# Optimization experiments

Hardware: AMD Instinct MI355X
Metric: run time of the kernel (lower is better)

## Reference

```python
import jax, jax.numpy as jnp
import numpy as np

D = 1024      # input_dim
H = 4096      # hidden_dim
E = 8         # expert_count
TOP_K = 2
N = 8192      # tokens
LN_EPS = 1e-5


def setup_inputs() -> dict:
    key = jax.random.key(0)
    ks = jax.random.split(key, 10)
    s_d = 1.0 / np.sqrt(D)
    s_h = 1.0 / np.sqrt(H)
    return {
        "x": jax.random.normal(ks[0], (N, D), dtype=jnp.float32),
        "ln_gamma": jnp.ones((D,), jnp.float32),
        "ln_beta": jnp.zeros((D,), jnp.float32),
        "conf_w": jax.random.uniform(ks[1], (D, 1), jnp.float32, -s_d, s_d),
        "conf_b": jnp.zeros((1,), jnp.float32),
        "router_w": jax.random.uniform(ks[2], (D, E), jnp.float32, -s_d, s_d),
        "router_b": jnp.zeros((E,), jnp.float32),
        "w1": jax.random.uniform(ks[3], (E, D, H), jnp.float32, -s_d, s_d),
        "b1": jax.random.uniform(ks[4], (E, H), jnp.float32, -s_d, s_d),
        "w2": jax.random.uniform(ks[5], (E, H, D), jnp.float32, -s_h, s_h),
        "b2": jax.random.uniform(ks[6], (E, D), jnp.float32, -s_h, s_h),
    }


def reference(x, ln_gamma, ln_beta, conf_w, conf_b, router_w, router_b, w1, b1, w2, b2):
    # LayerNorm (torch default eps=1e-5, affine)
    mu = jnp.mean(x, axis=-1, keepdims=True)
    var = jnp.mean(jnp.square(x - mu), axis=-1, keepdims=True)
    x_norm = (x - mu) * jax.lax.rsqrt(var + LN_EPS) * ln_gamma + ln_beta

    # layer-skip confidence head
    confidence = jax.nn.sigmoid(x_norm @ conf_w + conf_b)  # [N,1]

    # router: softmax -> top-k -> renormalize selected weights
    router_probs = jax.nn.softmax(x_norm @ router_w + router_b, axis=-1)  # [N,E]
    vals, indices = jax.lax.top_k(router_probs, TOP_K)                    # [N,K]
    vals = vals / jnp.sum(vals, axis=-1, keepdims=True)

    # scatter top-k weights into dense per-expert combine weights [N,E]
    combine_w = jnp.zeros((x.shape[0], E), x.dtype).at[
        jnp.arange(x.shape[0])[:, None], indices].add(vals)

    # dispatch/combine: loop over small fixed expert count (dense compute,
    # weighted by combine_w, mathematically identical to per-token dispatch)
    combined = jnp.zeros_like(x)
    for e in range(E):
        h = jax.nn.relu(x_norm @ w1[e] + b1[e])      # [N,H]
        combined = combined + combine_w[:, e:e + 1] * (h @ w2[e] + b2[e])

    output = x + combined
    return output, confidence, x
```

## Files before the change

kernel.cpp:

```cpp
#include <hip/hip_runtime.h>
#include <hip/hip_bf16.h>

#define N_TOK 8192
#define DIM   1024
#define HID   4096
#define NEXP  8
#define CSTR  64
#define RTMAX 136
#define HROWS 16896
#define EPS   264

using bf16x8 = __attribute__((ext_vector_type(8))) short;
using f32x4  = __attribute__((ext_vector_type(4))) float;

__device__ __forceinline__ void gload_lds16(const void* g, void* l) {
  __builtin_amdgcn_global_load_lds(
      (const __attribute__((address_space(1))) unsigned int*)g,
      (__attribute__((address_space(3))) unsigned int*)l, 16, 0, 0);
}

__device__ __forceinline__ float wredsum(float v) {
#pragma unroll
  for (int off = 32; off > 0; off >>= 1) v += __shfl_xor(v, off, 64);
  return v;
}

__device__ __forceinline__ unsigned short f2bf(float f) {
  __hip_bfloat16 h = __float2bfloat16(f);
  return *reinterpret_cast<unsigned short*>(&h);
}
__device__ __forceinline__ float bf2f(unsigned short u) {
  return __uint_as_float((unsigned)u << 16);
}

__device__ __forceinline__ void transpose_body(
    const float* __restrict__ src, __hip_bfloat16* __restrict__ dst,
    int R, int C, int c0, int r0, float (*tile)[65]) {
  const int tid = threadIdx.x;
  const int tx = tid & 15, ty = tid >> 4;
#pragma unroll
  for (int k = 0; k < 4; k++) {
    const int row = ty + k * 16;
    const float4 v = *(const float4*)(src + (size_t)(r0 + row) * C + c0 + tx * 4);
    tile[row][tx * 4 + 0] = v.x; tile[row][tx * 4 + 1] = v.y;
    tile[row][tx * 4 + 2] = v.z; tile[row][tx * 4 + 3] = v.w;
  }
  __syncthreads();
#pragma unroll
  for (int k = 0; k < 4; k++) {
    const int orow = ty + k * 16;
    ushort4 st;
    st.x = f2bf(tile[tx * 4 + 0][orow]);
    st.y = f2bf(tile[tx * 4 + 1][orow]);
    st.z = f2bf(tile[tx * 4 + 2][orow]);
    st.w = f2bf(tile[tx * 4 + 3][orow]);
    *(ushort4*)((unsigned short*)dst + (size_t)(c0 + orow) * R + r0 + tx * 4) = st;
  }
}

__global__ __launch_bounds__(256) void setup_kernel(
    const float* __restrict__ x, const float* __restrict__ gamma, const float* __restrict__ beta,
    const float* __restrict__ conf_w, const float* __restrict__ conf_b,
    const float* __restrict__ rw, const float* __restrict__ rb,
    const float* __restrict__ w1, const float* __restrict__ w2,
    __hip_bfloat16* __restrict__ w1t, __hip_bfloat16* __restrict__ w2t,
    __hip_bfloat16* __restrict__ xn, float* __restrict__ out,
    int* __restrict__ counts, int* __restrict__ lists, float* __restrict__ wts,
    int2* __restrict__ idx) {
  __shared__ float tile[64][65];
  const int b = (int)blockIdx.x;
  if (b < 8192) {
    const int z = b >> 10, r = b & 1023;
    const int cx = r & 63, ry = r >> 6;
    transpose_body(w1 + (size_t)z * DIM * HID, w1t + (size_t)z * DIM * HID,
                   DIM, HID, cx * 64, ry * 64, tile);
    return;
  }
  if (b < 16384) {
    const int bb = b - 8192;
    const int z = bb >> 10, r = bb & 1023;
    const int cx = r & 15, ry = r >> 4;
    transpose_body(w2 + (size_t)z * HID * DIM, w2t + (size_t)z * HID * DIM,
                   HID, DIM, cx * 64, ry * 64, tile);
    return;
  }
  const int t = (b - 16384) * 4 + ((int)threadIdx.x >> 6);
  const int lane = threadIdx.x & 63;
  const float* xr = x + (size_t)t * DIM;

  float4 xv[4];
#pragma unroll
  for (int q = 0; q < 4; q++) xv[q] = *(const float4*)(xr + q * 256 + lane * 4);

  float s = 0.f, s2 = 0.f;
#pragma unroll
  for (int q = 0; q < 4; q++) {
    s  += xv[q].x + xv[q].y + xv[q].z + xv[q].w;
    s2 += xv[q].x * xv[q].x + xv[q].y * xv[q].y + xv[q].z * xv[q].z + xv[q].w * xv[q].w;
  }
  s = wredsum(s); s2 = wredsum(s2);
  const float mu  = s * (1.f / DIM);
  const float inv = rsqrtf(s2 * (1.f / DIM) - mu * mu + 1e-5f);

  float p[9];
#pragma unroll
  for (int e = 0; e < 9; e++) p[e] = 0.f;

#pragma unroll
  for (int q = 0; q < 4; q++) {
    const int d0 = q * 256 + lane * 4;
    const float4 g4 = *(const float4*)(gamma + d0);
    const float4 b4 = *(const float4*)(beta + d0);
    float v0 = (xv[q].x - mu) * inv * g4.x + b4.x;
    float v1 = (xv[q].y - mu) * inv * g4.y + b4.y;
    float v2 = (xv[q].z - mu) * inv * g4.z + b4.z;
    float v3 = (xv[q].w - mu) * inv * g4.w + b4.w;

    ushort4 st; st.x = f2bf(v0); st.y = f2bf(v1); st.z = f2bf(v2); st.w = f2bf(v3);
    *(ushort4*)((unsigned short*)xn + (size_t)t * DIM + d0) = st;
    *(float4*)(out + (size_t)t * DIM + d0) = xv[q];
    *(float4*)(out + (size_t)N_TOK * DIM + N_TOK + (size_t)t * DIM + d0) = xv[q];

    const float vv[4] = {v0, v1, v2, v3};
#pragma unroll
    for (int j = 0; j < 4; j++) {
      const int d = d0 + j;
      const float v = vv[j];
      p[8] += v * conf_w[d];
      const float4 r0 = *(const float4*)(rw + d * 8);
      const float4 r1 = *(const float4*)(rw + d * 8 + 4);
      p[0] += v * r0.x; p[1] += v * r0.y; p[2] += v * r0.z; p[3] += v * r0.w;
      p[4] += v * r1.x; p[5] += v * r1.y; p[6] += v * r1.z; p[7] += v * r1.w;
    }
  }
#pragma unroll
  for (int e = 0; e < 9; e++) p[e] = wredsum(p[e]);

  if (lane == 0) {
    float L[8];
#pragma unroll
    for (int e = 0; e < 8; e++) L[e] = p[e] + rb[e];
    const float cl = p[8] + conf_b[0];
    out[(size_t)N_TOK * DIM + t] = 1.f / (1.f + expf(-cl));

    float mx = L[0];
#pragma unroll
    for (int e = 1; e < 8; e++) mx = fmaxf(mx, L[e]);
    float pe[8];
#pragma unroll
    for (int e = 0; e < 8; e++) pe[e] = expf(L[e] - mx);
    int i0 = 0; float v0 = pe[0];
#pragma unroll
    for (int e = 1; e < 8; e++) if (pe[e] > v0) { v0 = pe[e]; i0 = e; }
    int i1 = -1; float v1 = -1.f;
#pragma unroll
    for (int e = 0; e < 8; e++) if (e != i0 && pe[e] > v1) { v1 = pe[e]; i1 = e; }
    const float wsum = v0 + v1;
    const float w0 = v0 / wsum, w1v = v1 / wsum;
    int p0 = atomicAdd(&counts[i0 * CSTR], 1);
    lists[i0 * N_TOK + p0] = t; wts[i0 * N_TOK + p0] = w0;
    int p1 = atomicAdd(&counts[i1 * CSTR], 1);
    lists[i1 * N_TOK + p1] = t; wts[i1 * N_TOK + p1] = w1v;
    idx[t] = make_int2((i0 << 13) | p0, (i1 << 13) | p1);
  }
}

__global__ void bases_kernel(const int* __restrict__ counts, int* __restrict__ bases,
                             int* __restrict__ meta) {
  if (threadIdx.x == 0) {
    int s = 0, r = 0;
#pragma unroll
    for (int e = 0; e < NEXP; e++) {
      bases[e] = s; meta[e] = r;
      const int c = counts[e * CSTR];
      s += c; r += (c + 127) >> 7;
    }
    meta[NEXP] = r;
  }
}


#define GEMM_CORE(NT)                                                                   \
  f32x4 acc[4][4] = {};                                                                 \
  stage(0, 0); stage(1, 24576);                                                         \
  for (int t = 0; t < (NT); ++t) {                                                      \
    const int pb = (t % 3) * 24576;                                                     \
    if (t + 1 < (NT)) { asm volatile("s_waitcnt vmcnt(3)" ::: "memory"); }              \
    else              { asm volatile("s_waitcnt vmcnt(0)" ::: "memory"); }              \
    __builtin_amdgcn_s_barrier();                                                       \
    if (t + 2 < (NT)) stage(t + 2, ((t + 2) % 3) * 24576);                              \
    const char* Ab = smem + pb + Abase;                                                 \
    const char* Bb = smem + pb + Bbase;                                                 \
    bf16x8 bfr[4], afr[4];                                                              \
    _Pragma("unroll")                                                                   \
    for (int n = 0; n < 4; n++) bfr[n] = *(const bf16x8*)(Bb + n * 1024);               \
    _Pragma("unroll")                                                                   \
    for (int m = 0; m < 4; m++) afr[m] = *(const bf16x8*)(Ab + m * 1024);               \
    asm volatile("s_waitcnt lgkmcnt(0)" ::: "memory");                                  \
    __builtin_amdgcn_sched_barrier(0);                                                  \
    __builtin_amdgcn_s_setprio(1);                                                      \
    _Pragma("unroll")                                                                   \
    for (int m = 0; m < 4; m++)                                                         \
      _Pragma("unroll")                                                                 \
      for (int n = 0; n < 4; n++)                                                       \
        acc[m][n] = __builtin_amdgcn_mfma_f32_16x16x32_bf16(afr[m], bfr[n], acc[m][n], 0, 0, 0); \
    __builtin_amdgcn_s_setprio(0);                                                      \
  }

#define DECODE_BLOCK(PPX)                                                     \
  int panel, rtg;                                                             \
  if ((PPX) > 0) {                                                            \
    const int x_ = (int)blockIdx.x & 7;                                       \
    const int q_ = (int)blockIdx.x >> 3;                                      \
    rtg = q_ / (PPX);                                                         \
    panel = x_ * (PPX) + (q_ - rtg * (PPX));                                  \
  } else {                                                                    \
    panel = (int)blockIdx.x / RTMAX;                                          \
    rtg = (int)blockIdx.x - panel * RTMAX;                                    \
  }                                                                           \
  if (rtg >= meta[NEXP]) return;                                              \
  int e = 0;                                                                  \
  _Pragma("unroll")                                                           \
  for (int k = 1; k < NEXP; k++) if (meta[k] <= rtg) e = k;                   \
  const int rt = rtg - meta[e];                                               \
  const int cnt = counts[e * CSTR];                                           \
  const int hbase = bases[e];

#define GEMM_COMMON()                                                         \
  __shared__ char smem[73728];                                                \
  const int tid = threadIdx.x;                                                \
  const int l = tid & 63;                                                     \
  const int w8 = tid >> 6;                                                    \
  const int wr = w8 >> 2;                                                     \
  const int wc = w8 & 3;                                                      \
  const int lr = l & 15;                                                      \
  const int pchunk = (l >> 4) ^ ((lr >> 1) & 3);                              \
  const int Abase = (wr * 64 + lr) * 64 + pchunk * 16;                        \
  const int Bbase = 8192 + (wc * 64 + lr) * 64 + pchunk * 16;                 \
  const int srow = tid >> 2;                      \
  const int lc = (tid & 3) ^ ((srow >> 1) & 3);

#define EPILOGUE(EXPR, DSTROW)                                                \
  __builtin_amdgcn_s_barrier();                                               \
  {                                                                           \
    unsigned short* ep = (unsigned short*)smem;                               \
    _Pragma("unroll")                                                         \
    for (int n = 0; n < 4; n++) {                                             \
      const int col = wc * 64 + n * 16 + lr;                                  \
      _Pragma("unroll")                                                       \
      for (int m = 0; m < 4; m++) {                                           \
        f32x4 v = acc[m][n];                                                  \
        _Pragma("unroll")                                                     \
        for (int j = 0; j < 4; j++) {                                         \
          const int row = wr * 64 + m * 16 + (l >> 4) * 4 + j;                \
          ep[row * EPS + col] = (EXPR);                                       \
        }                                                                     \
      }                                                                       \
    }                                                                         \
    asm volatile("s_waitcnt lgkmcnt(0)" ::: "memory");                        \
    __builtin_amdgcn_s_barrier();                                             \
    const int g = tid >> 5, u = tid & 31;                                     \
    _Pragma("unroll")                                                         \
    for (int i = 0; i < 8; i++) {                                             \
      const int row = i * 16 + g;                                             \
      const int pos = rt * 128 + row;                                         \
      if (pos < cnt) {                                                        \
        bf16x8 vv = *(const bf16x8*)(ep + row * EPS + u * 8);                 \
        *(bf16x8*)(DSTROW + u * 8) = vv;                                      \
      }                                                                       \
    }                                                                         \
  }

__global__ __launch_bounds__(512, 4) void gemm1_kernel(
    const __hip_bfloat16* __restrict__ xn, const __hip_bfloat16* __restrict__ w1t_b,
    const float* __restrict__ b1, const int* __restrict__ lists,
    const int* __restrict__ counts, const int* __restrict__ bases,
    const int* __restrict__ meta, __hip_bfloat16* __restrict__ hbuf, const int ppx) {
  DECODE_BLOCK(ppx)
  const int ct = panel;
  const int* list = lists + e * N_TOK;
  const __hip_bfloat16* w1t = w1t_b + (size_t)e * DIM * HID;
  GEMM_COMMON()

  const int apos = rt * 128 + srow;
  const int tok = list[apos < cnt ? apos : 0];
  const unsigned short* srcA0 = (const unsigned short*)xn + (size_t)tok * DIM + lc * 8;
  const unsigned short* srcB0 = (const unsigned short*)w1t + (size_t)(ct * 256 + srow) * DIM + lc * 8;
  const unsigned short* srcB1 = (const unsigned short*)w1t + (size_t)(ct * 256 + 128 + srow) * DIM + lc * 8;

  auto stage = [&](int tt, int lbase) {
    gload_lds16(srcA0 + tt * 32, smem + lbase + tid * 16);
    gload_lds16(srcB0 + tt * 32, smem + lbase + 8192 + tid * 16);
    gload_lds16(srcB1 + tt * 32, smem + lbase + 16384 + tid * 16);
  };

  GEMM_CORE(DIM / 32)

  const float bv[4] = {
    b1[e * HID + ct * 256 + wc * 64 + 0 * 16 + lr],
    b1[e * HID + ct * 256 + wc * 64 + 1 * 16 + lr],
    b1[e * HID + ct * 256 + wc * 64 + 2 * 16 + lr],
    b1[e * HID + ct * 256 + wc * 64 + 3 * 16 + lr]};
#pragma unroll
  for (int n = 0; n < 4; n++)
#pragma unroll
    for (int m = 0; m < 4; m++)
#pragma unroll
      for (int j = 0; j < 4; j++) acc[m][n][j] = fmaxf(acc[m][n][j] + bv[n], 0.f);
  EPILOGUE(f2bf(v[j]),
           (unsigned short*)hbuf + (size_t)(hbase + pos) * HID + ct * 256)
}

__global__ __launch_bounds__(512, 4) void gemm2_kernel(
    const __hip_bfloat16* __restrict__ hbuf, const __hip_bfloat16* __restrict__ w2t_b,
    const int* __restrict__ counts, const int* __restrict__ bases,
    const int* __restrict__ meta, __hip_bfloat16* __restrict__ ybuf,
    const int SK, const int ppx) {
  DECODE_BLOCK(ppx)
  const int ct = panel & 3;
  const int ksp = panel >> 2;
  const int kbase = ksp * (HID / SK);
  const __hip_bfloat16* w2t = w2t_b + (size_t)e * DIM * HID;
  GEMM_COMMON()

  const unsigned short* srcA0 = (const unsigned short*)hbuf +
      (size_t)(hbase + rt * 128 + srow) * HID + kbase + lc * 8;
  const unsigned short* srcB0 = (const unsigned short*)w2t +
      (size_t)(ct * 256 + srow) * HID + kbase + lc * 8;
  const unsigned short* srcB1 = (const unsigned short*)w2t +
      (size_t)(ct * 256 + 128 + srow) * HID + kbase + lc * 8;

  auto stage = [&](int tt, int lbase) {
    gload_lds16(srcA0 + tt * 32, smem + lbase + tid * 16);
    gload_lds16(srcB0 + tt * 32, smem + lbase + 8192 + tid * 16);
    gload_lds16(srcB1 + tt * 32, smem + lbase + 16384 + tid * 16);
  };

  const int nk = (HID / 32) / SK;
  GEMM_CORE(nk)

  EPILOGUE(f2bf(v[j]),
           (unsigned short*)ybuf + ((size_t)ksp * HROWS + hbase + pos) * DIM + ct * 256)
}

__global__ __launch_bounds__(256) void combine_kernel(
    const __hip_bfloat16* __restrict__ ybuf, const float* __restrict__ b2,
    const int2* __restrict__ idx, const float* __restrict__ wv,
    const int* __restrict__ bases, float* __restrict__ out, const int SK) {
  const int t = blockIdx.x * 4 + (threadIdx.x >> 6);
  const int lane = threadIdx.x & 63;
  const int2 iv = idx[t];
  const int e0 = iv.x >> 13, p0 = iv.x & (N_TOK - 1);
  const int e1 = iv.y >> 13, p1 = iv.y & (N_TOK - 1);
  const float w0 = wv[iv.x], w1 = wv[iv.y];
  const int r0 = bases[e0] + p0;
  const int r1 = bases[e1] + p1;
#pragma unroll
  for (int q = 0; q < 4; q++) {
    const int d0 = q * 256 + lane * 4;
    float4 o = *(const float4*)(out + (size_t)t * DIM + d0);
    float y0x = 0.f, y0y = 0.f, y0z = 0.f, y0w = 0.f;
    float y1x = 0.f, y1y = 0.f, y1z = 0.f, y1w = 0.f;
    for (int s = 0; s < SK; s++) {
      const ushort4 a = *(const ushort4*)((const unsigned short*)ybuf +
                          ((size_t)s * HROWS + r0) * DIM + d0);
      const ushort4 b = *(const ushort4*)((const unsigned short*)ybuf +
                          ((size_t)s * HROWS + r1) * DIM + d0);
      y0x += bf2f(a.x); y0y += bf2f(a.y); y0z += bf2f(a.z); y0w += bf2f(a.w);
      y1x += bf2f(b.x); y1y += bf2f(b.y); y1z += bf2f(b.z); y1w += bf2f(b.w);
    }
    const float4 bb0 = *(const float4*)(b2 + e0 * DIM + d0);
    const float4 bb1 = *(const float4*)(b2 + e1 * DIM + d0);
    o.x += w0 * (y0x + bb0.x) + w1 * (y1x + bb1.x);
    o.y += w0 * (y0y + bb0.y) + w1 * (y1y + bb1.y);
    o.z += w0 * (y0z + bb0.z) + w1 * (y1z + bb1.z);
    o.w += w0 * (y0w + bb0.w) + w1 * (y1w + bb1.w);
    *(float4*)(out + (size_t)t * DIM + d0) = o;
  }
}

extern "C" void kernel_launch(void* const* d_in, const int* in_sizes, int n_in,
                              void* d_out, int out_size, void* d_ws, size_t ws_size,
                              hipStream_t stream) {
  (void)in_sizes; (void)n_in; (void)out_size;
  const float* x      = (const float*)d_in[0];
  const float* gamma  = (const float*)d_in[1];
  const float* beta   = (const float*)d_in[2];
  const float* conf_w = (const float*)d_in[3];
  const float* conf_b = (const float*)d_in[4];
  const float* rw     = (const float*)d_in[5];
  const float* rb     = (const float*)d_in[6];
  const float* w1     = (const float*)d_in[7];
  const float* b1     = (const float*)d_in[8];
  const float* w2     = (const float*)d_in[9];
  const float* b2     = (const float*)d_in[10];
  float* out = (float*)d_out;

  char* w = (char*)d_ws;
  auto alloc = [&](size_t bytes) { char* p = w; w += (bytes + 255) & ~255ULL; return p; };

  __hip_bfloat16* xn = (__hip_bfloat16*)alloc((size_t)N_TOK * DIM * 2);
  int*   lists  = (int*)alloc((size_t)NEXP * N_TOK * 4);
  float* wtsb   = (float*)alloc((size_t)NEXP * N_TOK * 4);
  int*   counts = (int*)alloc(NEXP * CSTR * 4);
  int*   bases  = (int*)alloc(256);
  int*   meta   = (int*)alloc(256);
  int2*  idx    = (int2*)alloc((size_t)N_TOK * 8);

  const size_t hbufA = (size_t)HROWS * HID * 2;
  const size_t wtA   = (size_t)NEXP * DIM * HID * 2;
  __hip_bfloat16* hbuf = (__hip_bfloat16*)alloc(hbufA);
  __hip_bfloat16* w1t  = (__hip_bfloat16*)alloc(wtA);
  __hip_bfloat16* w2t  = (__hip_bfloat16*)alloc(wtA);
  const size_t used = (size_t)(w - (char*)d_ws);
  const size_t ybuf1 = (size_t)HROWS * DIM * 2;

  int SK;
  __hip_bfloat16* ybuf;
  if (ws_size >= used + 2 * ybuf1 + 4096) {
    SK = 2; ybuf = (__hip_bfloat16*)alloc(2 * ybuf1);
  } else {
    SK = 1; ybuf = w1t;
  }
  const int g2ppx = (SK == 2) ? 1 : 0;
  const int g2grid = g2ppx > 0 ? 8 * g2ppx * RTMAX : 4 * RTMAX;

  hipMemsetAsync(counts, 0, NEXP * CSTR * 4, stream);
  setup_kernel<<<16384 + N_TOK / 4, 256, 0, stream>>>(
      x, gamma, beta, conf_w, conf_b, rw, rb, w1, w2, w1t, w2t,
      xn, out, counts, lists, wtsb, idx);
  bases_kernel<<<1, 64, 0, stream>>>(counts, bases, meta);
  gemm1_kernel<<<8 * 2 * RTMAX, 512, 0, stream>>>(xn, w1t, b1, lists, counts, bases, meta,
                                                  hbuf, 2);
  gemm2_kernel<<<g2grid, 512, 0, stream>>>(hbuf, w2t, counts, bases, meta, ybuf, SK, g2ppx);
  combine_kernel<<<N_TOK / 4, 256, 0, stream>>>(ybuf, b2, idx, wtsb, bases, out, SK);
}
```

Measured before the change: 494.4 us.

## Interleave LDS fragment loads with MFMAs and remap gemm2 block order

Result: no change. 487.2 us (-1.5%).

```diff
diff --git a/kernel.cpp b/kernel.cpp
--- a/kernel.cpp
+++ b/kernel.cpp
@@ -180,6 +180,17 @@
 }
 
 
+#define LGKM_SB(N)                                                            \
+  asm volatile("s_waitcnt lgkmcnt(" #N ")" ::: "memory");                     \
+  __builtin_amdgcn_sched_barrier(0);
+
+#define MFMA_G(MI, N0, NN)                                                    \
+  __builtin_amdgcn_s_setprio(1);                                              \
+  _Pragma("unroll")                                                           \
+  for (int n = (N0); n < (N0) + (NN); n++)                                    \
+    acc[MI][n] = __builtin_amdgcn_mfma_f32_16x16x32_bf16(afr[MI], bfr[n], acc[MI][n], 0, 0, 0); \
+  __builtin_amdgcn_s_setprio(0);
+
 #define GEMM_CORE(NT)                                                                   \
   f32x4 acc[4][4] = {};                                                                 \
   stage(0, 0); stage(1, 24576);                                                         \
@@ -192,32 +203,29 @@
     const char* Ab = smem + pb + Abase;                                                 \
     const char* Bb = smem + pb + Bbase;                                                 \
     bf16x8 bfr[4], afr[4];                                                              \
-    _Pragma("unroll")                                                                   \
-    for (int n = 0; n < 4; n++) bfr[n] = *(const bf16x8*)(Bb + n * 1024);               \
-    _Pragma("unroll")                                                                   \
-    for (int m = 0; m < 4; m++) afr[m] = *(const bf16x8*)(Ab + m * 1024);               \
-    asm volatile("s_waitcnt lgkmcnt(0)" ::: "memory");                                  \
-    __builtin_amdgcn_sched_barrier(0);                                                  \
-    __builtin_amdgcn_s_setprio(1);                                                      \
-    _Pragma("unroll")                                                                   \
-    for (int m = 0; m < 4; m++)                                                         \
-      _Pragma("unroll")                                                                 \
-      for (int n = 0; n < 4; n++)                                                       \
-        acc[m][n] = __builtin_amdgcn_mfma_f32_16x16x32_bf16(afr[m], bfr[n], acc[m][n], 0, 0, 0); \
-    __builtin_amdgcn_s_setprio(0);                                                      \
-  }
-
-#define DECODE_BLOCK(PPX)                                                     \
-  int panel, rtg;                                                             \
-  if ((PPX) > 0) {                                                            \
-    const int x_ = (int)blockIdx.x & 7;                                       \
-    const int q_ = (int)blockIdx.x >> 3;                                      \
-    rtg = q_ / (PPX);                                                         \
-    panel = x_ * (PPX) + (q_ - rtg * (PPX));                                  \
-  } else {                                                                    \
-    panel = (int)blockIdx.x / RTMAX;                                          \
-    rtg = (int)blockIdx.x - panel * RTMAX;                                    \
-  }                                                                           \
+    afr[0] = *(const bf16x8*)(Ab);                                                      \
+    bfr[0] = *(const bf16x8*)(Bb);                                                      \
+    bfr[1] = *(const bf16x8*)(Bb + 1024);                                               \
+    __builtin_amdgcn_sched_barrier(0);                                                  \
+    bfr[2] = *(const bf16x8*)(Bb + 2048);                                               \
+    __builtin_amdgcn_sched_barrier(0);                                                  \
+    bfr[3] = *(const bf16x8*)(Bb + 3072);                                               \
+    __builtin_amdgcn_sched_barrier(0);                                                  \
+    afr[1] = *(const bf16x8*)(Ab + 1024);                                               \
+    __builtin_amdgcn_sched_barrier(0);                                                  \
+    afr[2] = *(const bf16x8*)(Ab + 2048);                                               \
+    __builtin_amdgcn_sched_barrier(0);                                                  \
+    afr[3] = *(const bf16x8*)(Ab + 3072);                                               \
+    __builtin_amdgcn_sched_barrier(0);                                                  \
+    LGKM_SB(5) MFMA_G(0, 0, 2)                                                          \
+    LGKM_SB(4) MFMA_G(0, 2, 1)                                                          \
+    LGKM_SB(3) MFMA_G(0, 3, 1)                                                          \
+    LGKM_SB(2) MFMA_G(1, 0, 4)                                                          \
+    LGKM_SB(1) MFMA_G(2, 0, 4)                                                          \
+    LGKM_SB(0) MFMA_G(3, 0, 4)                                                          \
+  }
+
+#define DECODE_TAIL()                                                         \
   if (rtg >= meta[NEXP]) return;                                              \
   int e = 0;                                                                  \
   _Pragma("unroll")                                                           \
@@ -237,10 +245,10 @@
   const int pchunk = (l >> 4) ^ ((lr >> 1) & 3);                              \
   const int Abase = (wr * 64 + lr) * 64 + pchunk * 16;                        \
   const int Bbase = 8192 + (wc * 64 + lr) * 64 + pchunk * 16;                 \
-  const int srow = tid >> 2;                      \
+  const int srow = tid >> 2;                                                  \
   const int lc = (tid & 3) ^ ((srow >> 1) & 3);
 
-#define EPILOGUE(EXPR, DSTROW)                                                \
+#define EPILOGUE(DSTROW)                                                      \
   __builtin_amdgcn_s_barrier();                                               \
   {                                                                           \
     unsigned short* ep = (unsigned short*)smem;                               \
@@ -253,7 +261,7 @@
         _Pragma("unroll")                                                     \
         for (int j = 0; j < 4; j++) {                                         \
           const int row = wr * 64 + m * 16 + (l >> 4) * 4 + j;                \
-          ep[row * EPS + col] = (EXPR);                                       \
+          ep[row * EPS + col] = f2bf(v[j]);                                   \
         }                                                                     \
       }                                                                       \
     }                                                                         \
@@ -275,8 +283,12 @@
     const __hip_bfloat16* __restrict__ xn, const __hip_bfloat16* __restrict__ w1t_b,
     const float* __restrict__ b1, const int* __restrict__ lists,
     const int* __restrict__ counts, const int* __restrict__ bases,
-    const int* __restrict__ meta, __hip_bfloat16* __restrict__ hbuf, const int ppx) {
-  DECODE_BLOCK(ppx)
+    const int* __restrict__ meta, __hip_bfloat16* __restrict__ hbuf) {
+  const int x_ = (int)blockIdx.x & 7;
+  const int q_ = (int)blockIdx.x >> 3;
+  const int rtg = q_ >> 1;
+  const int panel = x_ * 2 + (q_ & 1);
+  DECODE_TAIL()
   const int ct = panel;
   const int* list = lists + e * N_TOK;
   const __hip_bfloat16* w1t = w1t_b + (size_t)e * DIM * HID;
@@ -307,16 +319,24 @@
     for (int m = 0; m < 4; m++)
 #pragma unroll
       for (int j = 0; j < 4; j++) acc[m][n][j] = fmaxf(acc[m][n][j] + bv[n], 0.f);
-  EPILOGUE(f2bf(v[j]),
-           (unsigned short*)hbuf + (size_t)(hbase + pos) * HID + ct * 256)
+  EPILOGUE((unsigned short*)hbuf + (size_t)(hbase + pos) * HID + ct * 256)
 }
 
 __global__ __launch_bounds__(512, 4) void gemm2_kernel(
     const __hip_bfloat16* __restrict__ hbuf, const __hip_bfloat16* __restrict__ w2t_b,
     const int* __restrict__ counts, const int* __restrict__ bases,
-    const int* __restrict__ meta, __hip_bfloat16* __restrict__ ybuf,
-    const int SK, const int ppx) {
-  DECODE_BLOCK(ppx)
+    const int* __restrict__ meta, __hip_bfloat16* __restrict__ ybuf, const int SK) {
+  int panel, rtg;
+  if (SK == 2) {
+    const int x_ = (int)blockIdx.x & 7;
+    const int q_ = (int)blockIdx.x >> 3;
+    rtg = (q_ >> 2) * 4 + (x_ >> 1);
+    panel = (x_ & 1) * 4 + (q_ & 3);
+  } else {
+    panel = (int)blockIdx.x / RTMAX;
+    rtg = (int)blockIdx.x - panel * RTMAX;
+  }
+  DECODE_TAIL()
   const int ct = panel & 3;
   const int ksp = panel >> 2;
   const int kbase = ksp * (HID / SK);
@@ -339,8 +359,7 @@
   const int nk = (HID / 32) / SK;
   GEMM_CORE(nk)
 
-  EPILOGUE(f2bf(v[j]),
-           (unsigned short*)ybuf + ((size_t)ksp * HROWS + hbase + pos) * DIM + ct * 256)
+  EPILOGUE((unsigned short*)ybuf + ((size_t)ksp * HROWS + hbase + pos) * DIM + ct * 256)
 }
 
 __global__ __launch_bounds__(256) void combine_kernel(
@@ -422,8 +441,7 @@
   } else {
     SK = 1; ybuf = w1t;
   }
-  const int g2ppx = (SK == 2) ? 1 : 0;
-  const int g2grid = g2ppx > 0 ? 8 * g2ppx * RTMAX : 4 * RTMAX;
+  const int g2grid = (SK == 2) ? 8 * RTMAX : 4 * RTMAX;
 
   hipMemsetAsync(counts, 0, NEXP * CSTR * 4, stream);
   setup_kernel<<<16384 + N_TOK / 4, 256, 0, stream>>>(
@@ -431,7 +449,7 @@
       xn, out, counts, lists, wtsb, idx);
   bases_kernel<<<1, 64, 0, stream>>>(counts, bases, meta);
   gemm1_kernel<<<8 * 2 * RTMAX, 512, 0, stream>>>(xn, w1t, b1, lists, counts, bases, meta,
-                                                  hbuf, 2);
-  gemm2_kernel<<<g2grid, 512, 0, stream>>>(hbuf, w2t, counts, bases, meta, ybuf, SK, g2ppx);
+                                                  hbuf);
+  gemm2_kernel<<<g2grid, 512, 0, stream>>>(hbuf, w2t, counts, bases, meta, ybuf, SK);
   combine_kernel<<<N_TOK / 4, 256, 0, stream>>>(ybuf, b2, idx, wtsb, bases, out, SK);
 }
```
